# Kernel tuning notes

Measured on AMD Instinct MI355X. Metric: run time of the kernel, lower is better.

## Reference

```python
import jax, jax.numpy as jnp
import numpy as np

N = 100_000; E = 3_200_000; F = 128; HID = 64; L = 4; H = 4; HD = 16; EMB = 64


def _ln(x, g, b):
    m = x.mean(-1, keepdims=True)
    v = ((x - m) ** 2).mean(-1, keepdims=True)
    return (x - m) / jnp.sqrt(v + 1e-5) * g + b


def _gelu(x):
    return jax.nn.gelu(x, approximate=False)


def _gat(h, src, dst, invalid, Wl, al, Wo):
    # Wl: (H, HID, HD), al: (H, 2*HD), Wo: (H*HD, HID)
    hh = jnp.einsum('nf,hfd->hnd', h, Wl)          # (H, N, HD)
    hs = hh[:, src]                                 # (H, E, HD) gather
    hd = hh[:, dst]                                 # (H, E, HD) gather
    e = jnp.einsum('hed,hd->he', hs, al[:, :HD]) + jnp.einsum('hed,hd->he', hd, al[:, HD:])
    e = jnp.where(e >= 0, e, 0.2 * e)               # LeakyReLU(0.2)
    e = jnp.where(invalid[None, :], -jnp.inf, e)
    seg_max = jax.vmap(lambda v: jax.ops.segment_max(v, dst, num_segments=N))(e)
    seg_max = jnp.where(jnp.isfinite(seg_max), seg_max, 0.0)  # empty segments -> 0 (matches include_self=False init 0)
    alpha = jnp.exp(jnp.minimum(e - seg_max[:, dst], 20.0))
    alpha = jnp.where(invalid[None, :], 0.0, alpha)
    asum = jax.vmap(lambda v: jax.ops.segment_sum(v, dst, num_segments=N))(alpha)
    an = alpha / (asum[:, dst] + 1e-8)
    msg = an[..., None] * hs                        # (H, E, HD)
    agg = jax.vmap(lambda m: jax.ops.segment_sum(m, dst, num_segments=N))(msg)  # (H, N, HD)
    return agg.transpose(1, 0, 2).reshape(N, H * HD) @ Wo


def setup_inputs() -> dict:
    key = jax.random.key(0)
    ks = jax.random.split(key, 20)
    rn = lambda k, shape, s: jax.random.normal(k, shape, jnp.float32) * s
    return {
        'node_features': jax.random.normal(ks[0], (N, F), jnp.float32),
        'edge_index': jax.random.randint(ks[1], (2, E), 0, N),
        'mask': jnp.ones((N,), bool),
        'ln_in_g': jnp.ones((F,), jnp.float32), 'ln_in_b': jnp.zeros((F,), jnp.float32),
        'W_in': rn(ks[2], (F, HID), 0.08), 'b_in': jnp.zeros((HID,), jnp.float32),
        'Wg': rn(ks[3], (L, H, HID, HD), 0.12),
        'attn': rn(ks[4], (L, H, 2 * HD), 0.2),
        'Wout': rn(ks[5], (L, H * HD, HID), 0.12),
        'norm_g': jnp.ones((L, HID), jnp.float32), 'norm_b': jnp.zeros((L, HID), jnp.float32),
        'We1': rn(ks[6], (HID, HID), 0.12), 'be1': jnp.zeros((HID,), jnp.float32),
        'We2': rn(ks[7], (HID, EMB), 0.12), 'be2': jnp.zeros((EMB,), jnp.float32),
        'Wrp': rn(ks[8], (HID, HID // 2), 0.12), 'brp': jnp.zeros((HID // 2,), jnp.float32),
        'Wro': rn(ks[9], (HID // 2, 1), 0.15), 'bro': jnp.zeros((1,), jnp.float32),
        'Wrs': rn(ks[10], (HID, 1), 0.12),
    }


def reference(node_features, edge_index, mask, ln_in_g, ln_in_b, W_in, b_in, Wg, attn, Wout,
              norm_g, norm_b, We1, be1, We2, be2, Wrp, brp, Wro, bro, Wrs):
    src, dst = edge_index[0], edge_index[1]
    invalid = ~mask[src]
    # input projection (dropout = eval identity)
    h = _gelu(_ln(node_features, ln_in_g, ln_in_b) @ W_in + b_in)
    for l in range(L):
        h = _ln(h + _gat(h, src, dst, invalid, Wg[l], attn[l], Wout[l]), norm_g[l], norm_b[l])
    hv = h  # mask is all-True so h[mask] == h (static shape)
    emb = jnp.tanh(_gelu(hv @ We1 + be1) @ We2 + be2)
    proj = _gelu(hv @ Wrp + brp)
    pred = (proj @ Wro + bro + hv @ Wrs)[:, 0]
    return pred, emb
```

## Files before the change

### kernel.cpp

```cpp
#include <hip/hip_runtime.h>
#include <hip/hip_bf16.h>
#include <hip/hip_fp16.h>
#include <math.h>

#define N_NODES 100000
#define E_EDGES 3200000
#define NQUADS  25000
#define LAYERS  4
#define DEGPAD  16

__device__ __forceinline__ float gelu_f(float x) {
    return 0.5f * x * (1.0f + erff(x * 0.70710678118654752f));
}
__device__ __forceinline__ float dot4(float4 a, float4 b) {
    return a.x * b.x + a.y * b.y + a.z * b.z + a.w * b.w;
}
__device__ __forceinline__ float4 fma4(float s, float4 w, float4 a) {
    a.x += s * w.x; a.y += s * w.y; a.z += s * w.z; a.w += s * w.w;
    return a;
}


__global__ void k_count(const int4* __restrict__ dst4, int* __restrict__ deg,
                        int4* __restrict__ rank4, int E4) {
    int i = blockIdx.x * blockDim.x + threadIdx.x;
    if (i < E4) {
        int4 d = dst4[i];
        int4 r;
        r.x = atomicAdd(&deg[d.x * DEGPAD], 1);
        r.y = atomicAdd(&deg[d.y * DEGPAD], 1);
        r.z = atomicAdd(&deg[d.z * DEGPAD], 1);
        r.w = atomicAdd(&deg[d.w * DEGPAD], 1);
        rank4[i] = r;
    }
}

__global__ __launch_bounds__(1024) void k_scan1(const int* __restrict__ deg,
        int* __restrict__ off, int* __restrict__ bsum, int n) {
    __shared__ int wsum[16];
    int lane = threadIdx.x & 63, wid = threadIdx.x >> 6;
    int i = blockIdx.x * 1024 + threadIdx.x;
    int v = (i < n) ? deg[(size_t)i * DEGPAD] : 0;
    int x = v;
    #pragma unroll
    for (int s = 1; s < 64; s <<= 1) {
        int t = __shfl_up(x, s, 64);
        if (lane >= s) x += t;
    }
    if (lane == 63) wsum[wid] = x;
    __syncthreads();
    int woff = 0;
    for (int w = 0; w < wid; ++w) woff += wsum[w];
    x += woff;
    if (i < n) off[i + 1] = x;
    if (threadIdx.x == 1023) bsum[blockIdx.x] = x;
}

__global__ void k_scan2(const int* __restrict__ bsum, int* __restrict__ bexc, int nb) {
    __shared__ int w0sum;
    int lane = threadIdx.x & 63, wid = threadIdx.x >> 6;
    int v = ((int)threadIdx.x < nb) ? bsum[threadIdx.x] : 0;
    int x = v;
    #pragma unroll
    for (int s = 1; s < 64; s <<= 1) {
        int t = __shfl_up(x, s, 64);
        if (lane >= s) x += t;
    }
    if (wid == 0 && lane == 63) w0sum = x;
    __syncthreads();
    int incl = x + (wid ? w0sum : 0);
    if ((int)threadIdx.x < nb) bexc[threadIdx.x] = incl - v;
}

__global__ void k_scan3(int* __restrict__ off, const int* __restrict__ bexc, int n) {
    int i = blockIdx.x * blockDim.x + threadIdx.x;
    if (i == 0) off[0] = 0;
    if (i < n) off[i + 1] += bexc[i >> 10];
}

__global__ void k_scatter(const int4* __restrict__ src4, const int4* __restrict__ dst4,
                          const int* __restrict__ off, const int4* __restrict__ rank4,
                          int* __restrict__ csr_src, int E4) {
    int i = blockIdx.x * blockDim.x + threadIdx.x;
    if (i < E4) {
        int4 s = src4[i];
        int4 d = dst4[i];
        int4 r = rank4[i];
        csr_src[off[d.x] + r.x] = s.x;
        csr_src[off[d.y] + r.y] = s.y;
        csr_src[off[d.z] + r.z] = s.z;
        csr_src[off[d.w] + r.w] = s.w;
    }
}


__global__ __launch_bounds__(256) void k_input(const float4* __restrict__ x4,
        const float4* __restrict__ g4, const float4* __restrict__ b4,
        const float4* __restrict__ Win4, const float4* __restrict__ bin4,
        float4* __restrict__ h4) {
    __shared__ float4 WL[128 * 16];
    __shared__ float4 gb[64];
    __shared__ float4 binL[16];
    __shared__ float4 hLw[4][4][33];
    for (int j = threadIdx.x; j < 2048; j += 256) WL[j] = Win4[j];
    if (threadIdx.x < 32) gb[threadIdx.x] = g4[threadIdx.x];
    else if (threadIdx.x < 64) gb[threadIdx.x] = b4[threadIdx.x - 32];
    else if (threadIdx.x < 80) binL[threadIdx.x - 64] = bin4[threadIdx.x - 64];
    __syncthreads();
    int lane = threadIdx.x & 63, wid = threadIdx.x >> 6;
    int c = lane & 15, n = lane >> 4;
    int gw = blockIdx.x * 4 + wid, nw = gridDim.x * 4;
    for (int quad = gw; quad < NQUADS; quad += nw) {
        int node = quad * 4 + n;
        float4 xa = x4[(size_t)node * 32 + c];
        float4 xb = x4[(size_t)node * 32 + 16 + c];
        float s = xa.x + xa.y + xa.z + xa.w + xb.x + xb.y + xb.z + xb.w;
        #pragma unroll
        for (int m = 8; m >= 1; m >>= 1) s += __shfl_xor(s, m, 64);
        float mean = s * (1.0f / 128.0f);
        float4 da = make_float4(xa.x - mean, xa.y - mean, xa.z - mean, xa.w - mean);
        float4 db = make_float4(xb.x - mean, xb.y - mean, xb.z - mean, xb.w - mean);
        float v = dot4(da, da) + dot4(db, db);
        #pragma unroll
        for (int m = 8; m >= 1; m >>= 1) v += __shfl_xor(v, m, 64);
        float rstd = rsqrtf(v * (1.0f / 128.0f) + 1e-5f);
        float4 ga = gb[c], gc = gb[c + 16], ba = gb[32 + c], bc = gb[48 + c];
        float4 na = make_float4(da.x * rstd * ga.x + ba.x, da.y * rstd * ga.y + ba.y,
                                da.z * rstd * ga.z + ba.z, da.w * rstd * ga.w + ba.w);
        float4 nb = make_float4(db.x * rstd * gc.x + bc.x, db.y * rstd * gc.y + bc.y,
                                db.z * rstd * gc.z + bc.z, db.w * rstd * gc.w + bc.w);
        hLw[wid][n][c] = na;
        hLw[wid][n][c + 16] = nb;
        float4 acc = binL[c];
        #pragma unroll 4
        for (int k4 = 0; k4 < 32; ++k4) {
            float4 xq = hLw[wid][n][k4];
            float4 w0 = WL[(k4 * 4 + 0) * 16 + c];
            float4 w1 = WL[(k4 * 4 + 1) * 16 + c];
            float4 w2 = WL[(k4 * 4 + 2) * 16 + c];
            float4 w3 = WL[(k4 * 4 + 3) * 16 + c];
            acc = fma4(xq.x, w0, acc);
            acc = fma4(xq.y, w1, acc);
            acc = fma4(xq.z, w2, acc);
            acc = fma4(xq.w, w3, acc);
        }
        float4 o = make_float4(gelu_f(acc.x), gelu_f(acc.y), gelu_f(acc.z), gelu_f(acc.w));
        h4[(size_t)quad * 64 + lane] = o;
    }
}


__global__ __launch_bounds__(256) void k_transform(const float4* __restrict__ h4,
        const float* __restrict__ Wg, const float4* __restrict__ al4,
        __half* __restrict__ hh, float* __restrict__ ssrc, float* __restrict__ sdst) {
    __shared__ float4 WL[64 * 16];
    __shared__ float4 aL[32];
    __shared__ float4 hLw[4][4][17];
    for (int j = threadIdx.x; j < 4096; j += 256) {
        int h_ = j >> 10, rem = j & 1023;
        int k = rem >> 4, d = rem & 15;
        ((float*)WL)[k * 64 + h_ * 16 + d] = Wg[j];
    }
    if (threadIdx.x < 32) aL[threadIdx.x] = al4[threadIdx.x];
    __syncthreads();
    int lane = threadIdx.x & 63, wid = threadIdx.x >> 6;
    int c = lane & 15, n = lane >> 4;
    int head = c >> 2, q = c & 3;
    float4 aA = aL[head * 8 + q];
    float4 aB = aL[head * 8 + 4 + q];
    int gw = blockIdx.x * 4 + wid, nw = gridDim.x * 4;
    for (int quad = gw; quad < NQUADS; quad += nw) {
        int node = quad * 4 + n;
        hLw[wid][n][c] = h4[(size_t)quad * 64 + lane];
        float4 acc = make_float4(0.f, 0.f, 0.f, 0.f);
        #pragma unroll 4
        for (int k4 = 0; k4 < 16; ++k4) {
            float4 xq = hLw[wid][n][k4];
            float4 w0 = WL[(k4 * 4 + 0) * 16 + c];
            float4 w1 = WL[(k4 * 4 + 1) * 16 + c];
            float4 w2 = WL[(k4 * 4 + 2) * 16 + c];
            float4 w3 = WL[(k4 * 4 + 3) * 16 + c];
            acc = fma4(xq.x, w0, acc);
            acc = fma4(xq.y, w1, acc);
            acc = fma4(xq.z, w2, acc);
            acc = fma4(xq.w, w3, acc);
        }
        __half2 lo = __floats2half2_rn(acc.x, acc.y);
        __half2 hi = __floats2half2_rn(acc.z, acc.w);
        uint2 pk = make_uint2(*(unsigned*)&lo, *(unsigned*)&hi);
        *(uint2*)(hh + (size_t)node * 64 + 4 * c) = pk;
        float t1 = dot4(acc, aA);
        float t2 = dot4(acc, aB);
        t1 += __shfl_xor(t1, 1, 64); t1 += __shfl_xor(t1, 2, 64);
        t2 += __shfl_xor(t2, 1, 64); t2 += __shfl_xor(t2, 2, 64);
        if (q == 0) {
            ssrc[node * 4 + head] = t1;
            sdst[node * 4 + head] = t2;
        }
    }
}


__device__ __forceinline__ float4 wmax4(float4 v) {
    #pragma unroll
    for (int m = 32; m >= 1; m >>= 1) {
        v.x = fmaxf(v.x, __shfl_xor(v.x, m, 64));
        v.y = fmaxf(v.y, __shfl_xor(v.y, m, 64));
        v.z = fmaxf(v.z, __shfl_xor(v.z, m, 64));
        v.w = fmaxf(v.w, __shfl_xor(v.w, m, 64));
    }
    return v;
}
__device__ __forceinline__ float4 wsum4(float4 v) {
    #pragma unroll
    for (int m = 32; m >= 1; m >>= 1) {
        v.x += __shfl_xor(v.x, m, 64);
        v.y += __shfl_xor(v.y, m, 64);
        v.z += __shfl_xor(v.z, m, 64);
        v.w += __shfl_xor(v.w, m, 64);
    }
    return v;
}
__device__ __forceinline__ float sel4(float4 v, int hd) {
    float r = v.x;
    if (hd == 1) r = v.y;
    if (hd == 2) r = v.z;
    if (hd == 3) r = v.w;
    return r;
}
__device__ __forceinline__ float4 leaky4(float4 s, float4 d) {
    float ex = s.x + d.x, ey = s.y + d.y, ez = s.z + d.z, ew = s.w + d.w;
    return make_float4((ex >= 0.f) ? ex : 0.2f * ex, (ey >= 0.f) ? ey : 0.2f * ey,
                       (ez >= 0.f) ? ez : 0.2f * ez, (ew >= 0.f) ? ew : 0.2f * ew);
}

__global__ __launch_bounds__(256) void k_edge(const int* __restrict__ off,
        const int* __restrict__ csr_src, const float4* __restrict__ ssrc4,
        const float4* __restrict__ sdst4, const __half* __restrict__ hh,
        float4* __restrict__ agg4, int n) {
    __shared__ float pbuf[4][64][4];
    int lane = threadIdx.x & 63, wid = threadIdx.x >> 6;
    int node = blockIdx.x * 4 + wid;
    if (node >= n) return;
    int sub = lane >> 3;
    int dp  = lane & 7;
    int hd2 = dp >> 1;
    float4 sd = sdst4[node];
    int s0 = off[node], s1 = off[node + 1];
    if (s0 == s1) {
        if (sub == 0) {
            float4 z = make_float4(0.f, 0.f, 0.f, 0.f);
            agg4[(size_t)node * 16 + dp * 2]     = z;
            agg4[(size_t)node * 16 + dp * 2 + 1] = z;
        }
        return;
    }
    float4 m4   = make_float4(-INFINITY, -INFINITY, -INFINITY, -INFINITY);
    float4 sum4 = make_float4(0.f, 0.f, 0.f, 0.f);
    float a0=0.f,a1=0.f,a2=0.f,a3=0.f,a4=0.f,a5=0.f,a6=0.f,a7=0.f;
    const __half* hrow = hh + dp * 8;
    int idx = s0 + lane;
    int sn = 0;
    float4 e4 = make_float4(-INFINITY, -INFINITY, -INFINITY, -INFINITY);
    if (idx < s1) {
        sn = csr_src[idx];
        e4 = leaky4(ssrc4[sn], sd);
    }
    for (int base = s0; base < s1; base += 64) {
        int cnt = min(64, s1 - base);
        int snc = sn;
        float4 e4c = e4;
        int nidx = base + 64 + lane;
        sn = 0;
        e4 = make_float4(-INFINITY, -INFINITY, -INFINITY, -INFINITY);
        if (nidx < s1) {
            sn = csr_src[nidx];
            e4 = leaky4(ssrc4[sn], sd);
        }
        float4 cm = wmax4(e4c);
        float4 mn = make_float4(fmaxf(m4.x, cm.x), fmaxf(m4.y, cm.y),
                                fmaxf(m4.z, cm.z), fmaxf(m4.w, cm.w));
        float4 scv = make_float4(__expf(m4.x - mn.x), __expf(m4.y - mn.y),
                                 __expf(m4.z - mn.z), __expf(m4.w - mn.w));
        float4 p4 = make_float4(__expf(e4c.x - mn.x), __expf(e4c.y - mn.y),
                                __expf(e4c.z - mn.z), __expf(e4c.w - mn.w));
        float4 sp = wsum4(p4);
        sum4.x = sum4.x * scv.x + sp.x;
        sum4.y = sum4.y * scv.y + sp.y;
        sum4.z = sum4.z * scv.z + sp.z;
        sum4.w = sum4.w * scv.w + sp.w;
        m4 = mn;
        *(float4*)&pbuf[wid][lane][0] = p4;
        float scm = sel4(scv, hd2);
        a0*=scm; a1*=scm; a2*=scm; a3*=scm; a4*=scm; a5*=scm; a6*=scm; a7*=scm;
        int cnt8 = (cnt + 7) & ~7;
        int j = 0;
        for (; j + 16 <= cnt8; j += 16) {
            int eA = j + sub, eB = j + 8 + sub;
            int sA = __shfl(snc, eA, 64);
            int sB = __shfl(snc, eB, 64);
            float wA = pbuf[wid][eA][hd2];
            float wB = pbuf[wid][eB][hd2];
            uint4 hA = *(const uint4*)(hrow + (size_t)sA * 64);
            uint4 hB = *(const uint4*)(hrow + (size_t)sB * 64);
            float2 f0 = __half22float2(*(__half2*)&hA.x);
            float2 f1 = __half22float2(*(__half2*)&hA.y);
            float2 f2 = __half22float2(*(__half2*)&hA.z);
            float2 f3 = __half22float2(*(__half2*)&hA.w);
            a0 += wA*f0.x; a1 += wA*f0.y; a2 += wA*f1.x; a3 += wA*f1.y;
            a4 += wA*f2.x; a5 += wA*f2.y; a6 += wA*f3.x; a7 += wA*f3.y;
            f0 = __half22float2(*(__half2*)&hB.x);
            f1 = __half22float2(*(__half2*)&hB.y);
            f2 = __half22float2(*(__half2*)&hB.z);
            f3 = __half22float2(*(__half2*)&hB.w);
            a0 += wB*f0.x; a1 += wB*f0.y; a2 += wB*f1.x; a3 += wB*f1.y;
            a4 += wB*f2.x; a5 += wB*f2.y; a6 += wB*f3.x; a7 += wB*f3.y;
        }
        for (; j < cnt8; j += 8) {
            int eA = j + sub;
            int sA = __shfl(snc, eA, 64);
            float wA = pbuf[wid][eA][hd2];
            uint4 hA = *(const uint4*)(hrow + (size_t)sA * 64);
            float2 f0 = __half22float2(*(__half2*)&hA.x);
            float2 f1 = __half22float2(*(__half2*)&hA.y);
            float2 f2 = __half22float2(*(__half2*)&hA.z);
            float2 f3 = __half22float2(*(__half2*)&hA.w);
            a0 += wA*f0.x; a1 += wA*f0.y; a2 += wA*f1.x; a3 += wA*f1.y;
            a4 += wA*f2.x; a5 += wA*f2.y; a6 += wA*f3.x; a7 += wA*f3.y;
        }
    }
    #pragma unroll
    for (int m = 8; m <= 32; m <<= 1) {
        a0 += __shfl_xor(a0, m, 64); a1 += __shfl_xor(a1, m, 64);
        a2 += __shfl_xor(a2, m, 64); a3 += __shfl_xor(a3, m, 64);
        a4 += __shfl_xor(a4, m, 64); a5 += __shfl_xor(a5, m, 64);
        a6 += __shfl_xor(a6, m, 64); a7 += __shfl_xor(a7, m, 64);
    }
    float inv = 1.0f / (sel4(sum4, hd2) + 1e-8f);
    if (sub == 0) {
        agg4[(size_t)node * 16 + dp * 2]     = make_float4(a0*inv, a1*inv, a2*inv, a3*inv);
        agg4[(size_t)node * 16 + dp * 2 + 1] = make_float4(a4*inv, a5*inv, a6*inv, a7*inv);
    }
}


__global__ __launch_bounds__(256) void k_out_tr(const float4* __restrict__ agg4,
        const float4* __restrict__ Wout4, float4* __restrict__ h4,
        const float4* __restrict__ ng4, const float4* __restrict__ nb4_,
        const float* __restrict__ Wg, const float4* __restrict__ al4,
        __half* __restrict__ hh, float* __restrict__ ssrc, float* __restrict__ sdst) {
    __shared__ float4 WL[64 * 16];
    __shared__ float4 WG[64 * 16];
    __shared__ float4 gnb[32];
    __shared__ float4 aL[32];
    __shared__ float4 hLw[4][4][17];
    for (int j = threadIdx.x; j < 1024; j += 256) WL[j] = Wout4[j];
    for (int j = threadIdx.x; j < 4096; j += 256) {
        int h_ = j >> 10, rem = j & 1023;
        int k = rem >> 4, d = rem & 15;
        ((float*)WG)[k * 64 + h_ * 16 + d] = Wg[j];
    }
    if (threadIdx.x < 16) gnb[threadIdx.x] = ng4[threadIdx.x];
    else if (threadIdx.x < 32) gnb[threadIdx.x] = nb4_[threadIdx.x - 16];
    else if (threadIdx.x < 64) aL[threadIdx.x - 32] = al4[threadIdx.x - 32];
    __syncthreads();
    int lane = threadIdx.x & 63, wid = threadIdx.x >> 6;
    int c = lane & 15, n = lane >> 4;
    int head = c >> 2, q = c & 3;
    float4 gg = gnb[c], bb = gnb[16 + c];
    float4 aA = aL[head * 8 + q];
    float4 aB = aL[head * 8 + 4 + q];
    int gw = blockIdx.x * 4 + wid, nw = gridDim.x * 4;
    for (int quad = gw; quad < NQUADS; quad += nw) {
        int node = quad * 4 + n;
        hLw[wid][n][c] = agg4[(size_t)quad * 64 + lane];
        float4 acc = make_float4(0.f, 0.f, 0.f, 0.f);
        #pragma unroll 4
        for (int k4 = 0; k4 < 16; ++k4) {
            float4 xq = hLw[wid][n][k4];
            float4 w0 = WL[(k4 * 4 + 0) * 16 + c];
            float4 w1 = WL[(k4 * 4 + 1) * 16 + c];
            float4 w2 = WL[(k4 * 4 + 2) * 16 + c];
            float4 w3 = WL[(k4 * 4 + 3) * 16 + c];
            acc = fma4(xq.x, w0, acc);
            acc = fma4(xq.y, w1, acc);
            acc = fma4(xq.z, w2, acc);
            acc = fma4(xq.w, w3, acc);
        }
        float4 hv = h4[(size_t)quad * 64 + lane];
        float4 r = make_float4(acc.x + hv.x, acc.y + hv.y, acc.z + hv.z, acc.w + hv.w);
        float s = r.x + r.y + r.z + r.w;
        #pragma unroll
        for (int m = 8; m >= 1; m >>= 1) s += __shfl_xor(s, m, 64);
        float mean = s * (1.f / 64.f);
        float4 d = make_float4(r.x - mean, r.y - mean, r.z - mean, r.w - mean);
        float v = dot4(d, d);
        #pragma unroll
        for (int m = 8; m >= 1; m >>= 1) v += __shfl_xor(v, m, 64);
        float rstd = rsqrtf(v * (1.f / 64.f) + 1e-5f);
        float4 o = make_float4(d.x * rstd * gg.x + bb.x, d.y * rstd * gg.y + bb.y,
                               d.z * rstd * gg.z + bb.z, d.w * rstd * gg.w + bb.w);
        h4[(size_t)quad * 64 + lane] = o;
        hLw[wid][n][c] = o;
        float4 acc2 = make_float4(0.f, 0.f, 0.f, 0.f);
        #pragma unroll 4
        for (int k4 = 0; k4 < 16; ++k4) {
            float4 xq = hLw[wid][n][k4];
            float4 w0 = WG[(k4 * 4 + 0) * 16 + c];
            float4 w1 = WG[(k4 * 4 + 1) * 16 + c];
            float4 w2 = WG[(k4 * 4 + 2) * 16 + c];
            float4 w3 = WG[(k4 * 4 + 3) * 16 + c];
            acc2 = fma4(xq.x, w0, acc2);
            acc2 = fma4(xq.y, w1, acc2);
            acc2 = fma4(xq.z, w2, acc2);
            acc2 = fma4(xq.w, w3, acc2);
        }
        __half2 lo = __floats2half2_rn(acc2.x, acc2.y);
        __half2 hi = __floats2half2_rn(acc2.z, acc2.w);
        uint2 pk = make_uint2(*(unsigned*)&lo, *(unsigned*)&hi);
        *(uint2*)(hh + (size_t)node * 64 + 4 * c) = pk;
        float t1 = dot4(acc2, aA);
        float t2 = dot4(acc2, aB);
        t1 += __shfl_xor(t1, 1, 64); t1 += __shfl_xor(t1, 2, 64);
        t2 += __shfl_xor(t2, 1, 64); t2 += __shfl_xor(t2, 2, 64);
        if (q == 0) {
            ssrc[node * 4 + head] = t1;
            sdst[node * 4 + head] = t2;
        }
    }
}


__global__ __launch_bounds__(256) void k_out(const float4* __restrict__ agg4,
        const float4* __restrict__ Wout4, float4* __restrict__ h4,
        const float4* __restrict__ ng4, const float4* __restrict__ nb4_) {
    __shared__ float4 WL[64 * 16];
    __shared__ float4 gnb[32];
    __shared__ float4 hLw[4][4][17];
    for (int j = threadIdx.x; j < 1024; j += 256) WL[j] = Wout4[j];
    if (threadIdx.x < 16) gnb[threadIdx.x] = ng4[threadIdx.x];
    else if (threadIdx.x < 32) gnb[threadIdx.x] = nb4_[threadIdx.x - 16];
    __syncthreads();
    int lane = threadIdx.x & 63, wid = threadIdx.x >> 6;
    int c = lane & 15, n = lane >> 4;
    float4 gg = gnb[c], bb = gnb[16 + c];
    int gw = blockIdx.x * 4 + wid, nw = gridDim.x * 4;
    for (int quad = gw; quad < NQUADS; quad += nw) {
        hLw[wid][n][c] = agg4[(size_t)quad * 64 + lane];
        float4 acc = make_float4(0.f, 0.f, 0.f, 0.f);
        #pragma unroll 4
        for (int k4 = 0; k4 < 16; ++k4) {
            float4 xq = hLw[wid][n][k4];
            float4 w0 = WL[(k4 * 4 + 0) * 16 + c];
            float4 w1 = WL[(k4 * 4 + 1) * 16 + c];
            float4 w2 = WL[(k4 * 4 + 2) * 16 + c];
            float4 w3 = WL[(k4 * 4 + 3) * 16 + c];
            acc = fma4(xq.x, w0, acc);
            acc = fma4(xq.y, w1, acc);
            acc = fma4(xq.z, w2, acc);
            acc = fma4(xq.w, w3, acc);
        }
        float4 hv = h4[(size_t)quad * 64 + lane];
        float4 r = make_float4(acc.x + hv.x, acc.y + hv.y, acc.z + hv.z, acc.w + hv.w);
        float s = r.x + r.y + r.z + r.w;
        #pragma unroll
        for (int m = 8; m >= 1; m >>= 1) s += __shfl_xor(s, m, 64);
        float mean = s * (1.f / 64.f);
        float4 d = make_float4(r.x - mean, r.y - mean, r.z - mean, r.w - mean);
        float v = dot4(d, d);
        #pragma unroll
        for (int m = 8; m >= 1; m >>= 1) v += __shfl_xor(v, m, 64);
        float rstd = rsqrtf(v * (1.f / 64.f) + 1e-5f);
        float4 o = make_float4(d.x * rstd * gg.x + bb.x, d.y * rstd * gg.y + bb.y,
                               d.z * rstd * gg.z + bb.z, d.w * rstd * gg.w + bb.w);
        h4[(size_t)quad * 64 + lane] = o;
    }
}


__global__ __launch_bounds__(256) void k_final(const float4* __restrict__ h4,
        const float4* __restrict__ We1_4, const float4* __restrict__ be1_4,
        const float4* __restrict__ We2_4, const float4* __restrict__ be2_4,
        const float4* __restrict__ Wrp_4, const float4* __restrict__ brp_4,
        const float4* __restrict__ Wro_4, const float* __restrict__ bro,
        const float4* __restrict__ Wrs_4,
        float* __restrict__ pred, float4* __restrict__ emb4) {
    __shared__ float4 W1L[64 * 16], W2L[64 * 16], WPL[64 * 8];
    __shared__ float4 be1L[16], be2L[16], brpL[8], wroL[8], wrsL[16];
    __shared__ float broL;
    __shared__ float4 hLw[4][4][17], uLw[4][4][17];
    for (int j = threadIdx.x; j < 1024; j += 256) { W1L[j] = We1_4[j]; W2L[j] = We2_4[j]; }
    for (int j = threadIdx.x; j < 512; j += 256) WPL[j] = Wrp_4[j];
    if (threadIdx.x < 16) be1L[threadIdx.x] = be1_4[threadIdx.x];
    else if (threadIdx.x < 32) be2L[threadIdx.x - 16] = be2_4[threadIdx.x - 16];
    else if (threadIdx.x < 40) brpL[threadIdx.x - 32] = brp_4[threadIdx.x - 32];
    else if (threadIdx.x < 48) wroL[threadIdx.x - 40] = Wro_4[threadIdx.x - 40];
    else if (threadIdx.x < 64) wrsL[threadIdx.x - 48] = Wrs_4[threadIdx.x - 48];
    if (threadIdx.x == 64) broL = bro[0];
    __syncthreads();
    int lane = threadIdx.x & 63, wid = threadIdx.x >> 6;
    int c = lane & 15, n = lane >> 4;
    int gw = blockIdx.x * 4 + wid, nw = gridDim.x * 4;
    for (int quad = gw; quad < NQUADS; quad += nw) {
        float4 hv = h4[(size_t)quad * 64 + lane];
        hLw[wid][n][c] = hv;
        float4 acc = be1L[c];
        #pragma unroll 4
        for (int k4 = 0; k4 < 16; ++k4) {
            float4 xq = hLw[wid][n][k4];
            float4 w0 = W1L[(k4 * 4 + 0) * 16 + c];
            float4 w1 = W1L[(k4 * 4 + 1) * 16 + c];
            float4 w2 = W1L[(k4 * 4 + 2) * 16 + c];
            float4 w3 = W1L[(k4 * 4 + 3) * 16 + c];
            acc = fma4(xq.x, w0, acc);
            acc = fma4(xq.y, w1, acc);
            acc = fma4(xq.z, w2, acc);
            acc = fma4(xq.w, w3, acc);
        }
        float4 u = make_float4(gelu_f(acc.x), gelu_f(acc.y), gelu_f(acc.z), gelu_f(acc.w));
        uLw[wid][n][c] = u;
        float4 acc2 = be2L[c];
        #pragma unroll 4
        for (int k4 = 0; k4 < 16; ++k4) {
            float4 xq = uLw[wid][n][k4];
            float4 w0 = W2L[(k4 * 4 + 0) * 16 + c];
            float4 w1 = W2L[(k4 * 4 + 1) * 16 + c];
            float4 w2 = W2L[(k4 * 4 + 2) * 16 + c];
            float4 w3 = W2L[(k4 * 4 + 3) * 16 + c];
            acc2 = fma4(xq.x, w0, acc2);
            acc2 = fma4(xq.y, w1, acc2);
            acc2 = fma4(xq.z, w2, acc2);
            acc2 = fma4(xq.w, w3, acc2);
        }
        float4 e = make_float4(tanhf(acc2.x), tanhf(acc2.y), tanhf(acc2.z), tanhf(acc2.w));
        emb4[(size_t)quad * 64 + lane] = e;
        float contrib = dot4(hv, wrsL[c]);
        if (c < 8) {
            float4 a3 = brpL[c];
            #pragma unroll 4
            for (int k4 = 0; k4 < 16; ++k4) {
                float4 xq = hLw[wid][n][k4];
                float4 w0 = WPL[(k4 * 4 + 0) * 8 + c];
                float4 w1 = WPL[(k4 * 4 + 1) * 8 + c];
                float4 w2 = WPL[(k4 * 4 + 2) * 8 + c];
                float4 w3 = WPL[(k4 * 4 + 3) * 8 + c];
                a3 = fma4(xq.x, w0, a3);
                a3 = fma4(xq.y, w1, a3);
                a3 = fma4(xq.z, w2, a3);
                a3 = fma4(xq.w, w3, a3);
            }
            float4 p = make_float4(gelu_f(a3.x), gelu_f(a3.y), gelu_f(a3.z), gelu_f(a3.w));
            contrib += dot4(p, wroL[c]);
        }
        #pragma unroll
        for (int m = 8; m >= 1; m >>= 1) contrib += __shfl_xor(contrib, m, 64);
        if (c == 0) pred[quad * 4 + n] = contrib + broL;
    }
}


extern "C" void kernel_launch(void* const* d_in, const int* in_sizes, int n_in,
                              void* d_out, int out_size, void* d_ws, size_t ws_size,
                              hipStream_t stream) {
    const float* node_features = (const float*)d_in[0];
    const int*   edge_index    = (const int*)d_in[1];
    const float* ln_in_g = (const float*)d_in[3];
    const float* ln_in_b = (const float*)d_in[4];
    const float* W_in    = (const float*)d_in[5];
    const float* b_in    = (const float*)d_in[6];
    const float* Wg      = (const float*)d_in[7];
    const float* attn    = (const float*)d_in[8];
    const float* Wout    = (const float*)d_in[9];
    const float* norm_g  = (const float*)d_in[10];
    const float* norm_b  = (const float*)d_in[11];
    const float* We1     = (const float*)d_in[12];
    const float* be1     = (const float*)d_in[13];
    const float* We2     = (const float*)d_in[14];
    const float* be2     = (const float*)d_in[15];
    const float* Wrp     = (const float*)d_in[16];
    const float* brp     = (const float*)d_in[17];
    const float* Wro     = (const float*)d_in[18];
    const float* bro     = (const float*)d_in[19];
    const float* Wrs     = (const float*)d_in[20];

    const int* src = edge_index;
    const int* dst = edge_index + E_EDGES;

    char* ws = (char*)d_ws;
    size_t o = 0;
    auto alloc = [&](size_t bytes) {
        void* p = ws + o;
        o += (bytes + 255) & ~(size_t)255;
        return p;
    };
    int*    off     = (int*)alloc((size_t)(N_NODES + 1) * 4);
    int*    rank    = (int*)alloc((size_t)E_EDGES * 4);
    int*    csr_src = (int*)alloc((size_t)E_EDGES * 4);
    float*  h       = (float*)alloc((size_t)N_NODES * 64 * 4);
    __half* hh      = (__half*)alloc((size_t)N_NODES * 64 * 2);
    float*  agg     = (float*)alloc((size_t)N_NODES * 64 * 4);
    float*  ssrc    = (float*)alloc((size_t)N_NODES * 4 * 4);
    float*  sdst    = (float*)alloc((size_t)N_NODES * 4 * 4);
    int*    bsum    = (int*)alloc(256 * 4);
    int*    bexc    = (int*)alloc(256 * 4);
    int*    deg     = (int*)agg;

    float* pred = (float*)d_out;
    float* emb  = (float*)d_out + N_NODES;

    hipMemsetAsync(deg, 0, (size_t)N_NODES * DEGPAD * 4, stream);

    int E4 = E_EDGES / 4;
    int eg4 = (E4 + 255) / 256;
    int nscan = (N_NODES + 1023) / 1024;
    k_count<<<eg4, 256, 0, stream>>>((const int4*)dst, deg, (int4*)rank, E4);
    k_scan1<<<nscan, 1024, 0, stream>>>(deg, off, bsum, N_NODES);
    k_scan2<<<1, 128, 0, stream>>>(bsum, bexc, nscan);
    k_scan3<<<(N_NODES + 255) / 256, 256, 0, stream>>>(off, bexc, N_NODES);
    k_scatter<<<eg4, 256, 0, stream>>>((const int4*)src, (const int4*)dst, off,
                                       (const int4*)rank, csr_src, E4);

    k_input<<<768, 256, 0, stream>>>((const float4*)node_features, (const float4*)ln_in_g,
                                     (const float4*)ln_in_b, (const float4*)W_in,
                                     (const float4*)b_in, (float4*)h);
    k_transform<<<1024, 256, 0, stream>>>((const float4*)h, Wg, (const float4*)attn,
                                          hh, ssrc, sdst);
    for (int l = 0; l < LAYERS; ++l) {
        k_edge<<<NQUADS, 256, 0, stream>>>(off, csr_src, (const float4*)ssrc,
                                           (const float4*)sdst, hh, (float4*)agg, N_NODES);
        if (l < LAYERS - 1) {
            k_out_tr<<<1024, 256, 0, stream>>>((const float4*)agg,
                    (const float4*)(Wout + l * 4096), (float4*)h,
                    (const float4*)(norm_g + l * 64), (const float4*)(norm_b + l * 64),
                    Wg + (l + 1) * 4096, (const float4*)(attn + (l + 1) * 128),
                    hh, ssrc, sdst);
        } else {
            k_out<<<1024, 256, 0, stream>>>((const float4*)agg,
                    (const float4*)(Wout + l * 4096), (float4*)h,
                    (const float4*)(norm_g + l * 64), (const float4*)(norm_b + l * 64));
        }
    }
    k_final<<<768, 256, 0, stream>>>((const float4*)h, (const float4*)We1, (const float4*)be1,
                                     (const float4*)We2, (const float4*)be2,
                                     (const float4*)Wrp, (const float4*)brp,
                                     (const float4*)Wro, bro, (const float4*)Wrs,
                                     pred, (float4*)emb);
}
```

Before: 853.9 us.

## Build CSR via per-block LDS histograms instead of global atomics; unroll edge gather

Replaces the global-atomic degree count with padded counters and the rank array by a two-phase blockwise counting sort: 64 blocks build per-block destination histograms in LDS over four bucket passes, a column scan produces per-block offsets, and a second pass scatters sources using LDS atomics. This removes the large memset, the rank buffer, and contended global atomics. The cost is only 64 blocks doing multiple passes over the edges, which may underuse the GPU. The edge aggregation loop is also unrolled to issue four gathered row loads per iteration for more memory-level parallelism.

```diff
diff --git a/kernel.cpp b/kernel.cpp
--- a/kernel.cpp
+++ b/kernel.cpp
@@ -7,7 +7,9 @@
 #define E_EDGES 3200000
 #define NQUADS  25000
 #define LAYERS  4
-#define DEGPAD  16
+#define NB_SORT 64
+#define PASSES  4
+#define BPP     25000
 
 __device__ __forceinline__ float gelu_f(float x) {
     return 0.5f * x * (1.0f + erff(x * 0.70710678118654752f));
@@ -21,18 +23,39 @@
 }
 
 
-__global__ void k_count(const int4* __restrict__ dst4, int* __restrict__ deg,
-                        int4* __restrict__ rank4, int E4) {
-    int i = blockIdx.x * blockDim.x + threadIdx.x;
-    if (i < E4) {
-        int4 d = dst4[i];
-        int4 r;
-        r.x = atomicAdd(&deg[d.x * DEGPAD], 1);
-        r.y = atomicAdd(&deg[d.y * DEGPAD], 1);
-        r.z = atomicAdd(&deg[d.z * DEGPAD], 1);
-        r.w = atomicAdd(&deg[d.w * DEGPAD], 1);
-        rank4[i] = r;
-    }
+__global__ __launch_bounds__(1024) void k_hist(const int* __restrict__ dst,
+        int* __restrict__ counts, int E) {
+    __shared__ int hcnt[BPP];
+    int b = blockIdx.x;
+    int chunk = (E + gridDim.x - 1) / gridDim.x;
+    int lo = b * chunk, hi = min(E, lo + chunk);
+    for (int p = 0; p < PASSES; ++p) {
+        int blo = p * BPP;
+        for (int j = threadIdx.x; j < BPP; j += 1024) hcnt[j] = 0;
+        __syncthreads();
+        for (int i = lo + (int)threadIdx.x; i < hi; i += 1024) {
+            int d = dst[i] - blo;
+            if ((unsigned)d < (unsigned)BPP) atomicAdd(&hcnt[d], 1);
+        }
+        __syncthreads();
+        int* out = counts + (size_t)b * N_NODES + blo;
+        for (int j = threadIdx.x; j < BPP; j += 1024) out[j] = hcnt[j];
+        __syncthreads();
+    }
+}
+
+__global__ void k_colscan(int* __restrict__ counts, int* __restrict__ deg, int n) {
+    int bucket = blockIdx.x * blockDim.x + threadIdx.x;
+    if (bucket >= n) return;
+    int run = 0;
+    #pragma unroll 4
+    for (int b = 0; b < NB_SORT; ++b) {
+        size_t idx = (size_t)b * N_NODES + bucket;
+        int t = counts[idx];
+        counts[idx] = run;
+        run += t;
+    }
+    deg[bucket] = run;
 }
 
 __global__ __launch_bounds__(1024) void k_scan1(const int* __restrict__ deg,
@@ -40,7 +63,7 @@
     __shared__ int wsum[16];
     int lane = threadIdx.x & 63, wid = threadIdx.x >> 6;
     int i = blockIdx.x * 1024 + threadIdx.x;
-    int v = (i < n) ? deg[(size_t)i * DEGPAD] : 0;
+    int v = (i < n) ? deg[i] : 0;
     int x = v;
     #pragma unroll
     for (int s = 1; s < 64; s <<= 1) {
@@ -78,18 +101,27 @@
     if (i < n) off[i + 1] += bexc[i >> 10];
 }
 
-__global__ void k_scatter(const int4* __restrict__ src4, const int4* __restrict__ dst4,
-                          const int* __restrict__ off, const int4* __restrict__ rank4,
-                          int* __restrict__ csr_src, int E4) {
-    int i = blockIdx.x * blockDim.x + threadIdx.x;
-    if (i < E4) {
-        int4 s = src4[i];
-        int4 d = dst4[i];
-        int4 r = rank4[i];
-        csr_src[off[d.x] + r.x] = s.x;
-        csr_src[off[d.y] + r.y] = s.y;
-        csr_src[off[d.z] + r.z] = s.z;
-        csr_src[off[d.w] + r.w] = s.w;
+__global__ __launch_bounds__(1024) void k_scat2(const int* __restrict__ dst,
+        const int* __restrict__ src, const int* __restrict__ off,
+        const int* __restrict__ counts, int* __restrict__ csr_src, int E) {
+    __shared__ int hcnt[BPP];
+    int b = blockIdx.x;
+    int chunk = (E + gridDim.x - 1) / gridDim.x;
+    int lo = b * chunk, hi = min(E, lo + chunk);
+    const int* myc = counts + (size_t)b * N_NODES;
+    for (int p = 0; p < PASSES; ++p) {
+        int blo = p * BPP;
+        for (int j = threadIdx.x; j < BPP; j += 1024) hcnt[j] = 0;
+        __syncthreads();
+        for (int i = lo + (int)threadIdx.x; i < hi; i += 1024) {
+            int d = dst[i];
+            int dl = d - blo;
+            if ((unsigned)dl < (unsigned)BPP) {
+                int lr = atomicAdd(&hcnt[dl], 1);
+                csr_src[off[d] + myc[d] + lr] = src[i];
+            }
+        }
+        __syncthreads();
     }
 }
 
@@ -233,6 +265,16 @@
     return make_float4((ex >= 0.f) ? ex : 0.2f * ex, (ey >= 0.f) ? ey : 0.2f * ey,
                        (ez >= 0.f) ? ez : 0.2f * ez, (ew >= 0.f) ? ew : 0.2f * ew);
 }
+__device__ __forceinline__ void acc8(float w, uint4 hv,
+        float& a0, float& a1, float& a2, float& a3,
+        float& a4, float& a5, float& a6, float& a7) {
+    float2 f0 = __half22float2(*(__half2*)&hv.x);
+    float2 f1 = __half22float2(*(__half2*)&hv.y);
+    float2 f2 = __half22float2(*(__half2*)&hv.z);
+    float2 f3 = __half22float2(*(__half2*)&hv.w);
+    a0 += w * f0.x; a1 += w * f0.y; a2 += w * f1.x; a3 += w * f1.y;
+    a4 += w * f2.x; a5 += w * f2.y; a6 += w * f3.x; a7 += w * f3.y;
+}
 
 __global__ __launch_bounds__(256) void k_edge(const int* __restrict__ off,
         const int* __restrict__ csr_src, const float4* __restrict__ ssrc4,
@@ -295,38 +337,31 @@
         a0*=scm; a1*=scm; a2*=scm; a3*=scm; a4*=scm; a5*=scm; a6*=scm; a7*=scm;
         int cnt8 = (cnt + 7) & ~7;
         int j = 0;
-        for (; j + 16 <= cnt8; j += 16) {
-            int eA = j + sub, eB = j + 8 + sub;
+        for (; j + 32 <= cnt8; j += 32) {
+            int eA = j + sub, eB = j + 8 + sub, eC = j + 16 + sub, eD = j + 24 + sub;
             int sA = __shfl(snc, eA, 64);
             int sB = __shfl(snc, eB, 64);
+            int sC = __shfl(snc, eC, 64);
+            int sD = __shfl(snc, eD, 64);
+            uint4 hA = *(const uint4*)(hrow + (size_t)sA * 64);
+            uint4 hB = *(const uint4*)(hrow + (size_t)sB * 64);
+            uint4 hC = *(const uint4*)(hrow + (size_t)sC * 64);
+            uint4 hD = *(const uint4*)(hrow + (size_t)sD * 64);
             float wA = pbuf[wid][eA][hd2];
             float wB = pbuf[wid][eB][hd2];
-            uint4 hA = *(const uint4*)(hrow + (size_t)sA * 64);
-            uint4 hB = *(const uint4*)(hrow + (size_t)sB * 64);
-            float2 f0 = __half22float2(*(__half2*)&hA.x);
-            float2 f1 = __half22float2(*(__half2*)&hA.y);
-            float2 f2 = __half22float2(*(__half2*)&hA.z);
-            float2 f3 = __half22float2(*(__half2*)&hA.w);
-            a0 += wA*f0.x; a1 += wA*f0.y; a2 += wA*f1.x; a3 += wA*f1.y;
-            a4 += wA*f2.x; a5 += wA*f2.y; a6 += wA*f3.x; a7 += wA*f3.y;
-            f0 = __half22float2(*(__half2*)&hB.x);
-            f1 = __half22float2(*(__half2*)&hB.y);
-            f2 = __half22float2(*(__half2*)&hB.z);
-            f3 = __half22float2(*(__half2*)&hB.w);
-            a0 += wB*f0.x; a1 += wB*f0.y; a2 += wB*f1.x; a3 += wB*f1.y;
-            a4 += wB*f2.x; a5 += wB*f2.y; a6 += wB*f3.x; a7 += wB*f3.y;
+            float wC = pbuf[wid][eC][hd2];
+            float wD = pbuf[wid][eD][hd2];
+            acc8(wA, hA, a0,a1,a2,a3,a4,a5,a6,a7);
+            acc8(wB, hB, a0,a1,a2,a3,a4,a5,a6,a7);
+            acc8(wC, hC, a0,a1,a2,a3,a4,a5,a6,a7);
+            acc8(wD, hD, a0,a1,a2,a3,a4,a5,a6,a7);
         }
         for (; j < cnt8; j += 8) {
             int eA = j + sub;
             int sA = __shfl(snc, eA, 64);
             float wA = pbuf[wid][eA][hd2];
             uint4 hA = *(const uint4*)(hrow + (size_t)sA * 64);
-            float2 f0 = __half22float2(*(__half2*)&hA.x);
-            float2 f1 = __half22float2(*(__half2*)&hA.y);
-            float2 f2 = __half22float2(*(__half2*)&hA.z);
-            float2 f3 = __half22float2(*(__half2*)&hA.w);
-            a0 += wA*f0.x; a1 += wA*f0.y; a2 += wA*f1.x; a3 += wA*f1.y;
-            a4 += wA*f2.x; a5 += wA*f2.y; a6 += wA*f3.x; a7 += wA*f3.y;
+            acc8(wA, hA, a0,a1,a2,a3,a4,a5,a6,a7);
         }
     }
     #pragma unroll
@@ -594,7 +629,6 @@
         return p;
     };
     int*    off     = (int*)alloc((size_t)(N_NODES + 1) * 4);
-    int*    rank    = (int*)alloc((size_t)E_EDGES * 4);
     int*    csr_src = (int*)alloc((size_t)E_EDGES * 4);
     float*  h       = (float*)alloc((size_t)N_NODES * 64 * 4);
     __half* hh      = (__half*)alloc((size_t)N_NODES * 64 * 2);
@@ -603,22 +637,19 @@
     float*  sdst    = (float*)alloc((size_t)N_NODES * 4 * 4);
     int*    bsum    = (int*)alloc(256 * 4);
     int*    bexc    = (int*)alloc(256 * 4);
-    int*    deg     = (int*)agg;
+    int*    counts  = (int*)agg;
+    int*    deg     = (int*)h;
 
     float* pred = (float*)d_out;
     float* emb  = (float*)d_out + N_NODES;
 
-    hipMemsetAsync(deg, 0, (size_t)N_NODES * DEGPAD * 4, stream);
-
-    int E4 = E_EDGES / 4;
-    int eg4 = (E4 + 255) / 256;
     int nscan = (N_NODES + 1023) / 1024;
-    k_count<<<eg4, 256, 0, stream>>>((const int4*)dst, deg, (int4*)rank, E4);
+    k_hist<<<NB_SORT, 1024, 0, stream>>>(dst, counts, E_EDGES);
+    k_colscan<<<(N_NODES + 255) / 256, 256, 0, stream>>>(counts, deg, N_NODES);
     k_scan1<<<nscan, 1024, 0, stream>>>(deg, off, bsum, N_NODES);
     k_scan2<<<1, 128, 0, stream>>>(bsum, bexc, nscan);
     k_scan3<<<(N_NODES + 255) / 256, 256, 0, stream>>>(off, bexc, N_NODES);
-    k_scatter<<<eg4, 256, 0, stream>>>((const int4*)src, (const int4*)dst, off,
-                                       (const int4*)rank, csr_src, E4);
+    k_scat2<<<NB_SORT, 1024, 0, stream>>>(dst, src, off, counts, csr_src, E_EDGES);
 
     k_input<<<768, 256, 0, stream>>>((const float4*)node_features, (const float4*)ln_in_g,
                                      (const float4*)ln_in_b, (const float4*)W_in,
```

Result: slower. 959.4 us (+12.4%).
